# Optimization experiments

Measured on AMD Instinct MI355X. Metric: run time of the kernel, lower is better.

Reference implementation:

```python
import jax, jax.numpy as jnp
import numpy as np

B, T, K, FT, FP, N, H, HEADS, C = 8, 5, 20, 384, 3, 128, 64, 8, 2
ALPHA = 0.2
NEG = -9e15


def gru(x, Wi, Wh, bi, bh):
    # x: [M, L, F] -> (full [M, L, Hd], last [M, Hd]); torch nn.GRU cell math
    Hd = Wh.shape[0]
    gx = jnp.einsum('mlf,fg->mlg', x, Wi) + bi  # precompute input projections

    def step(h, gxt):
        gh = h @ Wh + bh
        xr, xz, xn = jnp.split(gxt, 3, axis=-1)
        hr, hz, hn = jnp.split(gh, 3, axis=-1)
        r = jax.nn.sigmoid(xr + hr)
        z = jax.nn.sigmoid(xz + hz)
        n = jnp.tanh(xn + r * hn)
        h = (1. - z) * n + z * h
        return h, h

    h0 = jnp.zeros((x.shape[0], Hd), x.dtype)
    last, full = jax.lax.scan(step, h0, jnp.swapaxes(gx, 0, 1))
    return jnp.swapaxes(full, 0, 1), last


def temporal_attn(full, last):
    # attend over time using the last hidden state as the query
    a = jax.nn.softmax(jnp.einsum('mlh,mh->ml', full, last), axis=-1)
    return jnp.einsum('ml,mlh->mh', a, full)


def gat_forward(s, p, adj, sm1_Wi, sm1_Wh, sm1_bi, sm1_bh,
                sm2_Wi, sm2_Wh, sm2_bi, sm2_bh,
                pr_Wi, pr_Wh, pr_bi, pr_bh,
                Wb, bb, Wx, bx, W1, a1, W2, a2):
    mask = adj > 0  # [N, N]
    # --- SMEncoder: vectorized over (batch, stock, day) ---
    s_ = jnp.transpose(s, (0, 4, 1, 2, 3)).reshape(B * N * T, K, FT)
    f1, l1 = gru(s_, sm1_Wi, sm1_Wh, sm1_bi, sm1_bh)
    cv = temporal_attn(f1, l1).reshape(B * N, T, H)          # intra-day context
    f2, l2 = gru(cv, sm2_Wi, sm2_Wh, sm2_bi, sm2_bh)
    ct = temporal_attn(f2, l2).reshape(B, N, H)              # inter-day context
    # --- PriceEncoder: vectorized over (batch, stock) ---
    p_ = jnp.transpose(p, (0, 3, 1, 2)).reshape(B * N, T, FP)
    f3, l3 = gru(p_, pr_Wi, pr_Wh, pr_bi, pr_bh)
    qt = temporal_attn(f3, l3).reshape(B, N, H)
    # --- bilinear fusion + per-stock linear head (dropout is eval-mode identity) ---
    X = jnp.tanh(jnp.einsum('bni,oij,bnj->bno', ct, Wb, qt) + bb)   # [B, N, H]
    out1 = jnp.tanh(jnp.einsum('bnh,nch->bnc', X, Wx) + bx)          # [B, N, C]
    # --- multi-head GAT layer 1 (concat + LeakyReLU + adj-masked softmax) ---
    Whd = jnp.einsum('bnh,khf->bknf', X, W1)                         # [B, heads, N, H]
    e = jax.nn.leaky_relu(
        jnp.einsum('bknf,kf->bkn', Whd, a1[:, :H])[:, :, :, None]
        + jnp.einsum('bknf,kf->bkn', Whd, a1[:, H:])[:, :, None, :], ALPHA)
    att = jax.nn.softmax(jnp.where(mask, e, NEG), axis=-1)
    Xh = jax.nn.elu(jnp.einsum('bknm,bkmf->bknf', att, Whd))
    X2 = jnp.transpose(Xh, (0, 2, 1, 3)).reshape(B, N, HEADS * H)    # head concat
    # --- GAT layer 2 -> num_classes ---
    Wh2 = X2 @ W2                                                    # [B, N, C]
    e2 = jax.nn.leaky_relu((Wh2 @ a2[:C])[:, :, None]
                           + (Wh2 @ a2[C:])[:, None, :], ALPHA)
    att2 = jax.nn.softmax(jnp.where(mask, e2, NEG), axis=-1)
    Xo = jnp.einsum('bnm,bmc->bnc', att2, Wh2)
    return jnp.transpose(Xo + out1, (0, 2, 1))                       # [B, C, N]


def setup_inputs():
    key = jax.random.key(0)
    ks = jax.random.split(key, 23)
    g = lambda k, sh, sc=0.05: jax.random.normal(k, sh, jnp.float32) * sc
    adj = (jax.random.uniform(ks[2], (N, N)) < 0.3).astype(jnp.float32)
    adj = jnp.maximum(adj, jnp.eye(N, dtype=jnp.float32))
    return {
        's': jax.random.normal(ks[0], (B, T, K, FT, N), jnp.float32),
        'p': jax.random.normal(ks[1], (B, T, FP, N), jnp.float32),
        'adj': adj,
        'sm1_Wi': g(ks[3], (FT, 3 * H)), 'sm1_Wh': g(ks[4], (H, 3 * H)),
        'sm1_bi': g(ks[5], (3 * H,)), 'sm1_bh': g(ks[6], (3 * H,)),
        'sm2_Wi': g(ks[7], (H, 3 * H)), 'sm2_Wh': g(ks[8], (H, 3 * H)),
        'sm2_bi': g(ks[9], (3 * H,)), 'sm2_bh': g(ks[10], (3 * H,)),
        'pr_Wi': g(ks[11], (FP, 3 * H)), 'pr_Wh': g(ks[12], (H, 3 * H)),
        'pr_bi': g(ks[13], (3 * H,)), 'pr_bh': g(ks[14], (3 * H,)),
        'Wb': g(ks[15], (H, H, H)), 'bb': g(ks[16], (H,)),
        'Wx': g(ks[17], (N, C, H)), 'bx': g(ks[18], (N, C)),
        'W1': g(ks[19], (HEADS, H, H)), 'a1': g(ks[20], (HEADS, 2 * H)),
        'W2': g(ks[21], (HEADS * H, C)), 'a2': g(ks[22], (2 * C,)),
    }


def reference(s, p, adj, sm1_Wi, sm1_Wh, sm1_bi, sm1_bh,
              sm2_Wi, sm2_Wh, sm2_bi, sm2_bh,
              pr_Wi, pr_Wh, pr_bi, pr_bh,
              Wb, bb, Wx, bx, W1, a1, W2, a2):
    return gat_forward(s, p, adj, sm1_Wi, sm1_Wh, sm1_bi, sm1_bh,
                       sm2_Wi, sm2_Wh, sm2_bi, sm2_bh,
                       pr_Wi, pr_Wh, pr_bi, pr_bh,
                       Wb, bb, Wx, bx, W1, a1, W2, a2)
```

## Files before the change

kernel.cpp:

```cpp
#include <hip/hip_runtime.h>
#include <hip/hip_bf16.h>
#include <hip/hip_fp16.h>

#define DI __device__ __forceinline__

namespace {

constexpr int G_  = 192;
constexpr int FT_ = 384;
constexpr int M1_ = 5120;

typedef _Float16 f16x8 __attribute__((ext_vector_type(8)));
typedef _Float16 f16x4 __attribute__((ext_vector_type(4)));
typedef float    f32x4 __attribute__((ext_vector_type(4)));

DI float lrelu(float x) { return x > 0.f ? x : 0.2f * x; }
DI float sigmoidf(float x) { return 1.f / (1.f + __expf(-x)); }
DI float tanh_fast(float x) { float e = __expf(2.f * x); return 1.f - 2.f / (e + 1.f); }

__global__ __launch_bounds__(256) void k_cvtB(
    const float* __restrict__ Wi, _Float16* __restrict__ Bt) {
  int v = blockIdx.x * 256 + threadIdx.x;
  int g = v / 384, f = v % 384;
  Bt[v] = (_Float16)Wi[f * 192 + g];
}

__global__ __launch_bounds__(256) void k_gx1(
    const float* __restrict__ s, const _Float16* __restrict__ Bt,
    const float* __restrict__ bi, __half* __restrict__ gx1) {
  const int slab = blockIdx.x;
  const int b = slab / 100, rem = slab % 100, t = rem / 20, k = rem % 20;
  const float* A = s + (size_t)((b * 5 + t) * 20 + k) * (FT_ * 128);
  __shared__ __align__(16) _Float16 AsL[128 * 40];
  __shared__ __align__(16) _Float16 BsL[192 * 40];
  __shared__ float bisL[192];
  const int tid = threadIdx.x;
  if (tid < 192) bisL[tid] = bi[tid];
  const int w = tid >> 6, l = tid & 63;
  const int lr = l & 15, lk = l >> 4;

  f32x4 acc[12][2];
#pragma unroll
  for (int gt = 0; gt < 12; ++gt)
#pragma unroll
    for (int nt = 0; nt < 2; ++nt) acc[gt][nt] = (f32x4){0.f, 0.f, 0.f, 0.f};

  for (int kc = 0; kc < 12; ++kc) {
    const int f0 = kc * 32;
#pragma unroll
    for (int pass = 0; pass < 2; ++pass) {
      int task = tid + 256 * pass;
      int n = task & 127, oct = task >> 7;
      const float* src = A + (size_t)(f0 + oct * 8) * 128 + n;
      float v[8];
#pragma unroll
      for (int j = 0; j < 8; ++j) v[j] = src[j * 128];
      f16x8 h;
#pragma unroll
      for (int j = 0; j < 8; ++j) h[j] = (_Float16)v[j];
      *(f16x8*)&AsL[n * 40 + oct * 8] = h;
    }
#pragma unroll
    for (int pass = 0; pass < 3; ++pass) {
      int c = tid + 256 * pass;
      int g = c >> 2, oct = c & 3;
      f16x8 h = *(const f16x8*)&Bt[(size_t)g * 384 + f0 + oct * 8];
      *(f16x8*)&BsL[g * 40 + oct * 8] = h;
    }
    __syncthreads();
    f16x8 aN[2];
#pragma unroll
    for (int nt = 0; nt < 2; ++nt)
      aN[nt] = *(const f16x8*)&AsL[(w * 32 + nt * 16 + lr) * 40 + lk * 8];
#pragma unroll
    for (int gt = 0; gt < 12; ++gt) {
      f16x8 bW = *(const f16x8*)&BsL[(gt * 16 + lr) * 40 + lk * 8];
      acc[gt][0] = __builtin_amdgcn_mfma_f32_16x16x32_f16(bW, aN[0], acc[gt][0], 0, 0, 0);
      acc[gt][1] = __builtin_amdgcn_mfma_f32_16x16x32_f16(bW, aN[1], acc[gt][1], 0, 0, 0);
    }
    __syncthreads();
  }
#pragma unroll
  for (int nt = 0; nt < 2; ++nt) {
    int n = w * 32 + nt * 16 + lr;
    size_t m = (size_t)(b * 128 + n) * 5 + t;
    _Float16* dst = (_Float16*)gx1 + ((size_t)k * M1_ + m) * G_;
#pragma unroll
    for (int gt = 0; gt < 12; ++gt) {
      int gq = gt * 16 + lk * 4;
      float4 bias = *(const float4*)&bisL[gq];
      f32x4 c = acc[gt][nt];
      f16x4 h;
      h[0] = (_Float16)(c[0] + bias.x);
      h[1] = (_Float16)(c[1] + bias.y);
      h[2] = (_Float16)(c[2] + bias.z);
      h[3] = (_Float16)(c[3] + bias.w);
      *(f16x4*)&dst[gq] = h;
    }
  }
}

__global__ __launch_bounds__(192) void k_scan1(
    const __half* __restrict__ gx1, const float* __restrict__ Wh,
    const float* __restrict__ bh, float* __restrict__ cv) {
  const int s0 = blockIdx.x * 8;
  const int tid = threadIdx.x;
  __shared__ __align__(16) float hist[8][20][64];
  __shared__ float ghl[8][192];
  __shared__ float dls[8][20], als[8][20];
  float whcol[64];
#pragma unroll
  for (int i = 0; i < 64; ++i) whcol[i] = Wh[i * G_ + tid];
  const float bhg = bh[tid];

  for (int k = 0; k < 20; ++k) {
    if (k == 0) {
#pragma unroll
      for (int ss = 0; ss < 8; ++ss) ghl[ss][tid] = bhg;
    } else {
#pragma unroll
      for (int ss = 0; ss < 8; ++ss) {
        const float4* hq = (const float4*)&hist[ss][k - 1][0];
        float a = 0.f;
#pragma unroll
        for (int q = 0; q < 16; ++q) {
          float4 h4 = hq[q];
          a += h4.x * whcol[4 * q]     + h4.y * whcol[4 * q + 1]
             + h4.z * whcol[4 * q + 2] + h4.w * whcol[4 * q + 3];
        }
        ghl[ss][tid] = a + bhg;
      }
    }
    __syncthreads();
#pragma unroll
    for (int base = 0; base < 512; base += 192) {
      int task = base + tid;
      if (task < 512) {
        int ss = task >> 6, i = task & 63;
        size_t gbase = ((size_t)k * M1_ + (s0 + ss)) * G_;
        float xr = __half2float(gx1[gbase + i]);
        float xz = __half2float(gx1[gbase + 64 + i]);
        float xn = __half2float(gx1[gbase + 128 + i]);
        float hr = ghl[ss][i], hz = ghl[ss][64 + i], hn = ghl[ss][128 + i];
        float r  = sigmoidf(xr + hr);
        float z  = sigmoidf(xz + hz);
        float nn = tanh_fast(xn + r * hn);
        float hp = (k == 0) ? 0.f : hist[ss][k - 1][i];
        hist[ss][k][i] = (1.f - z) * nn + z * hp;
      }
    }
    __syncthreads();
  }
  if (tid < 160) {
    int ss = tid / 20, kk = tid % 20;
    float d = 0.f;
#pragma unroll
    for (int i = 0; i < 64; ++i) d += hist[ss][kk][i] * hist[ss][19][i];
    dls[ss][kk] = d;
  }
  __syncthreads();
  if (tid < 160) {
    int ss = tid / 20, kk = tid % 20;
    float mx = -3.4e38f;
#pragma unroll
    for (int j = 0; j < 20; ++j) mx = fmaxf(mx, dls[ss][j]);
    als[ss][kk] = __expf(dls[ss][kk] - mx);
  }
  __syncthreads();
  for (int idx = tid; idx < 512; idx += 192) {
    int ss = idx >> 6, i = idx & 63;
    float sum = 0.f, a = 0.f;
#pragma unroll
    for (int kk = 0; kk < 20; ++kk) sum += als[ss][kk];
#pragma unroll
    for (int kk = 0; kk < 20; ++kk) a += als[ss][kk] * hist[ss][kk][i];
    cv[(size_t)(s0 + ss) * 64 + i] = a / sum;
  }
}

__global__ __launch_bounds__(192) void k_scan2(
    const float* __restrict__ x, const float* __restrict__ Wi,
    const float* __restrict__ Wh, const float* __restrict__ bi,
    const float* __restrict__ bh, float* __restrict__ outv) {
  const int s0 = blockIdx.x * 4;
  const int tid = threadIdx.x;
  __shared__ __align__(16) float hist[4][5][64];
  __shared__ __align__(16) float xl[4][64];
  __shared__ float ghl[4][192], gxl[4][192];
  __shared__ float dls[4][5], als[4][5];
  float wic[64], whc[64];
#pragma unroll
  for (int i = 0; i < 64; ++i) { wic[i] = Wi[i * G_ + tid]; whc[i] = Wh[i * G_ + tid]; }
  const float big = bi[tid], bhg = bh[tid];

  for (int t = 0; t < 5; ++t) {
    for (int v = tid; v < 256; v += 192) {
      int ss = v >> 6, i = v & 63;
      xl[ss][i] = x[((size_t)(s0 + ss) * 5 + t) * 64 + i];
    }
    __syncthreads();
#pragma unroll
    for (int ss = 0; ss < 4; ++ss) {
      const float4* xq = (const float4*)&xl[ss][0];
      float ax = 0.f;
#pragma unroll
      for (int q = 0; q < 16; ++q) {
        float4 v4 = xq[q];
        ax += v4.x * wic[4 * q]     + v4.y * wic[4 * q + 1]
            + v4.z * wic[4 * q + 2] + v4.w * wic[4 * q + 3];
      }
      gxl[ss][tid] = ax + big;
      float ah = 0.f;
      if (t > 0) {
        const float4* hq = (const float4*)&hist[ss][t - 1][0];
#pragma unroll
        for (int q = 0; q < 16; ++q) {
          float4 h4 = hq[q];
          ah += h4.x * whc[4 * q]     + h4.y * whc[4 * q + 1]
              + h4.z * whc[4 * q + 2] + h4.w * whc[4 * q + 3];
        }
      }
      ghl[ss][tid] = ah + bhg;
    }
    __syncthreads();
    {
      int task = tid;
#pragma unroll
      for (int base = 0; base < 256; base += 192) {
        int tk = base + tid;
        if (tk < 256) {
          int ss = tk >> 6, i = tk & 63;
          float xr = gxl[ss][i], xz = gxl[ss][64 + i], xn = gxl[ss][128 + i];
          float hr = ghl[ss][i], hz = ghl[ss][64 + i], hn = ghl[ss][128 + i];
          float r  = sigmoidf(xr + hr);
          float z  = sigmoidf(xz + hz);
          float nn = tanh_fast(xn + r * hn);
          float hp = (t == 0) ? 0.f : hist[ss][t - 1][i];
          hist[ss][t][i] = (1.f - z) * nn + z * hp;
        }
      }
      (void)task;
    }
    __syncthreads();
  }
  if (tid < 20) {
    int ss = tid / 5, kk = tid % 5;
    float d = 0.f;
#pragma unroll
    for (int i = 0; i < 64; ++i) d += hist[ss][kk][i] * hist[ss][4][i];
    dls[ss][kk] = d;
  }
  __syncthreads();
  if (tid < 20) {
    int ss = tid / 5, kk = tid % 5;
    float mx = -3.4e38f;
#pragma unroll
    for (int j = 0; j < 5; ++j) mx = fmaxf(mx, dls[ss][j]);
    als[ss][kk] = __expf(dls[ss][kk] - mx);
  }
  __syncthreads();
  for (int idx = tid; idx < 256; idx += 192) {
    int ss = idx >> 6, i = idx & 63;
    float sum = 0.f, a = 0.f;
#pragma unroll
    for (int kk = 0; kk < 5; ++kk) sum += als[ss][kk];
#pragma unroll
    for (int kk = 0; kk < 5; ++kk) a += als[ss][kk] * hist[ss][kk][i];
    outv[(size_t)(s0 + ss) * 64 + i] = a / sum;
  }
}

__global__ __launch_bounds__(192) void k_scan3(
    const float* __restrict__ p, const float* __restrict__ Wi,
    const float* __restrict__ Wh, const float* __restrict__ bi,
    const float* __restrict__ bh, float* __restrict__ outv) {
  const int s0 = blockIdx.x * 4;
  const int tid = threadIdx.x;
  __shared__ __align__(16) float hist[4][5][64];
  __shared__ float xp[4][3];
  __shared__ float ghl[4][192], gxl[4][192];
  __shared__ float dls[4][5], als[4][5];
  float wic[3], whc[64];
#pragma unroll
  for (int f = 0; f < 3; ++f) wic[f] = Wi[f * G_ + tid];
#pragma unroll
  for (int i = 0; i < 64; ++i) whc[i] = Wh[i * G_ + tid];
  const float big = bi[tid], bhg = bh[tid];

  for (int t = 0; t < 5; ++t) {
    if (tid < 12) {
      int ss = tid / 3, f = tid % 3;
      int seq = s0 + ss, b = seq >> 7, n = seq & 127;
      xp[ss][f] = p[((size_t)(b * 5 + t) * 3 + f) * 128 + n];
    }
    __syncthreads();
#pragma unroll
    for (int ss = 0; ss < 4; ++ss) {
      gxl[ss][tid] = xp[ss][0] * wic[0] + xp[ss][1] * wic[1] + xp[ss][2] * wic[2] + big;
      float ah = 0.f;
      if (t > 0) {
        const float4* hq = (const float4*)&hist[ss][t - 1][0];
#pragma unroll
        for (int q = 0; q < 16; ++q) {
          float4 h4 = hq[q];
          ah += h4.x * whc[4 * q]     + h4.y * whc[4 * q + 1]
              + h4.z * whc[4 * q + 2] + h4.w * whc[4 * q + 3];
        }
      }
      ghl[ss][tid] = ah + bhg;
    }
    __syncthreads();
#pragma unroll
    for (int base = 0; base < 256; base += 192) {
      int tk = base + tid;
      if (tk < 256) {
        int ss = tk >> 6, i = tk & 63;
        float xr = gxl[ss][i], xz = gxl[ss][64 + i], xn = gxl[ss][128 + i];
        float hr = ghl[ss][i], hz = ghl[ss][64 + i], hn = ghl[ss][128 + i];
        float r  = sigmoidf(xr + hr);
        float z  = sigmoidf(xz + hz);
        float nn = tanh_fast(xn + r * hn);
        float hp = (t == 0) ? 0.f : hist[ss][t - 1][i];
        hist[ss][t][i] = (1.f - z) * nn + z * hp;
      }
    }
    __syncthreads();
  }
  if (tid < 20) {
    int ss = tid / 5, kk = tid % 5;
    float d = 0.f;
#pragma unroll
    for (int i = 0; i < 64; ++i) d += hist[ss][kk][i] * hist[ss][4][i];
    dls[ss][kk] = d;
  }
  __syncthreads();
  if (tid < 20) {
    int ss = tid / 5, kk = tid % 5;
    float mx = -3.4e38f;
#pragma unroll
    for (int j = 0; j < 5; ++j) mx = fmaxf(mx, dls[ss][j]);
    als[ss][kk] = __expf(dls[ss][kk] - mx);
  }
  __syncthreads();
  for (int idx = tid; idx < 256; idx += 192) {
    int ss = idx >> 6, i = idx & 63;
    float sum = 0.f, a = 0.f;
#pragma unroll
    for (int kk = 0; kk < 5; ++kk) sum += als[ss][kk];
#pragma unroll
    for (int kk = 0; kk < 5; ++kk) a += als[ss][kk] * hist[ss][kk][i];
    outv[(size_t)(s0 + ss) * 64 + i] = a / sum;
  }
}

__global__ __launch_bounds__(256) void k_bilinear(
    const float* __restrict__ ct, const float* __restrict__ qt,
    const float* __restrict__ Wb, const float* __restrict__ bb,
    float* __restrict__ X) {
  const int bn0 = blockIdx.x * 4;
  const int tid = threadIdx.x;
  __shared__ float ctl[4][64], qtl[4][64];
  {
    int ss = tid >> 6, i = tid & 63;
    ctl[ss][i] = ct[(size_t)(bn0 + ss) * 64 + i];
    qtl[ss][i] = qt[(size_t)(bn0 + ss) * 64 + i];
  }
  __syncthreads();
  const int o = tid >> 2, part = tid & 3, j0 = part << 4;
  float qr[4][16];
#pragma unroll
  for (int pp = 0; pp < 4; ++pp)
#pragma unroll
    for (int q = 0; q < 16; ++q) qr[pp][q] = qtl[pp][j0 + q];
  float acc[4] = {0.f, 0.f, 0.f, 0.f};
  const float* wb = Wb + (size_t)o * 4096 + j0;
  for (int i = 0; i < 64; ++i) {
    const float4* w4 = (const float4*)(wb + i * 64);
    float tmp[4] = {0.f, 0.f, 0.f, 0.f};
#pragma unroll
    for (int q = 0; q < 4; ++q) {
      float4 w = w4[q];
#pragma unroll
      for (int pp = 0; pp < 4; ++pp)
        tmp[pp] += w.x * qr[pp][4 * q]     + w.y * qr[pp][4 * q + 1]
                 + w.z * qr[pp][4 * q + 2] + w.w * qr[pp][4 * q + 3];
    }
#pragma unroll
    for (int pp = 0; pp < 4; ++pp) acc[pp] += ctl[pp][i] * tmp[pp];
  }
#pragma unroll
  for (int pp = 0; pp < 4; ++pp) {
    acc[pp] += __shfl_xor(acc[pp], 1);
    acc[pp] += __shfl_xor(acc[pp], 2);
  }
  if (part == 0) {
    float bbv = bb[o];
#pragma unroll
    for (int pp = 0; pp < 4; ++pp)
      X[(size_t)(bn0 + pp) * 64 + o] = tanh_fast(acc[pp] + bbv);
  }
}

__global__ __launch_bounds__(256) void k_gat1(
    const float* __restrict__ X, const float* __restrict__ W1,
    const float* __restrict__ a1, const float* __restrict__ adj,
    float* __restrict__ X2) {
  const int b = blockIdx.x >> 3, k = blockIdx.x & 7;
  const int tid = threadIdx.x;
  __shared__ __align__(16) float whd[128][68];
  __shared__ float w1l[64][64];
  __shared__ float d1l[128], d2l[128];
  for (int v = tid; v < 4096; v += 256) w1l[v >> 6][v & 63] = W1[(size_t)k * 4096 + v];
  __syncthreads();
  {
    const int f = tid & 63, ng = tid >> 6;
    const float* Xb = X + (size_t)b * 128 * 64;
    for (int n = ng * 32; n < ng * 32 + 32; ++n) {
      float a = 0.f;
#pragma unroll
      for (int h = 0; h < 64; ++h) a += Xb[n * 64 + h] * w1l[h][f];
      whd[n][f] = a;
    }
  }
  __syncthreads();
  if (tid < 128) {
    const int n = tid;
    float da = 0.f, db = 0.f;
#pragma unroll
    for (int f = 0; f < 64; ++f) {
      float w = whd[n][f];
      da += w * a1[k * 128 + f];
      db += w * a1[k * 128 + 64 + f];
    }
    d1l[n] = da; d2l[n] = db;
  }
  __syncthreads();
  {
    const int n = tid & 127, fh = tid >> 7;
    unsigned long long mlo = 0ull, mhi = 0ull;
    for (int m = 0; m < 64; ++m) if (adj[n * 128 + m] > 0.f)      mlo |= (1ull << m);
    for (int m = 0; m < 64; ++m) if (adj[n * 128 + 64 + m] > 0.f) mhi |= (1ull << m);
    const float d1n = d1l[n];
    float mx = -3.4e38f;
    for (int m = 0; m < 128; ++m) {
      bool on = (m < 64) ? (((mlo >> m) & 1ull) != 0) : (((mhi >> (m - 64)) & 1ull) != 0);
      float e = lrelu(d1n + d2l[m]);
      mx = fmaxf(mx, on ? e : -3.4e38f);
    }
    float sum = 0.f;
    float acc[32];
#pragma unroll
    for (int q = 0; q < 32; ++q) acc[q] = 0.f;
    for (int m = 0; m < 128; ++m) {
      bool on = (m < 64) ? (((mlo >> m) & 1ull) != 0) : (((mhi >> (m - 64)) & 1ull) != 0);
      float w = on ? __expf(lrelu(d1n + d2l[m]) - mx) : 0.f;
      sum += w;
      const float4* wr = (const float4*)&whd[m][fh * 32];
#pragma unroll
      for (int q8 = 0; q8 < 8; ++q8) {
        float4 wv = wr[q8];
        acc[4 * q8]     += w * wv.x;
        acc[4 * q8 + 1] += w * wv.y;
        acc[4 * q8 + 2] += w * wv.z;
        acc[4 * q8 + 3] += w * wv.w;
      }
    }
    float inv = 1.f / sum;
    float* dst = X2 + ((size_t)b * 128 + n) * 512 + k * 64 + fh * 32;
#pragma unroll
    for (int q = 0; q < 32; ++q) {
      float v = acc[q] * inv;
      dst[q] = v > 0.f ? v : (__expf(v) - 1.f);
    }
  }
}

__global__ __launch_bounds__(256) void k_head(
    const float* __restrict__ X, const float* __restrict__ Wx, const float* __restrict__ bx,
    const float* __restrict__ X2, const float* __restrict__ W2, const float* __restrict__ a2,
    const float* __restrict__ adj, float* __restrict__ out) {
  const int b = blockIdx.x;
  const int tid = threadIdx.x;
  __shared__ float w2l[1024];
  __shared__ float wh2l[128][2];
  __shared__ float d2aL[128], d2bL[128];
  __shared__ float out1L[128][2];
  for (int v = tid; v < 1024; v += 256) w2l[v] = W2[v];
  __syncthreads();
  const int w = tid >> 6, l = tid & 63;
  const float a20 = a2[0], a21 = a2[1], a22 = a2[2], a23 = a2[3];
  for (int it = 0; it < 32; ++it) {
    int n = w * 32 + it;
    const float* xr = X2 + ((size_t)b * 128 + n) * 512 + l * 8;
    float4 xa = *(const float4*)xr;
    float4 xb = *(const float4*)(xr + 4);
    float xs[8] = {xa.x, xa.y, xa.z, xa.w, xb.x, xb.y, xb.z, xb.w};
    float s0 = 0.f, s1 = 0.f;
#pragma unroll
    for (int j = 0; j < 8; ++j) {
      s0 += xs[j] * w2l[(l * 8 + j) * 2];
      s1 += xs[j] * w2l[(l * 8 + j) * 2 + 1];
    }
#pragma unroll
    for (int d = 1; d < 64; d <<= 1) { s0 += __shfl_xor(s0, d); s1 += __shfl_xor(s1, d); }
    if (l == 0) {
      wh2l[n][0] = s0; wh2l[n][1] = s1;
      d2aL[n] = s0 * a20 + s1 * a21;
      d2bL[n] = s0 * a22 + s1 * a23;
    }
  }
  if (tid < 128) {
    int n = tid;
    const float* xrow = X + ((size_t)b * 128 + n) * 64;
#pragma unroll
    for (int c = 0; c < 2; ++c) {
      float a = 0.f;
#pragma unroll
      for (int h = 0; h < 64; ++h) a += xrow[h] * Wx[(n * 2 + c) * 64 + h];
      out1L[n][c] = tanh_fast(a + bx[n * 2 + c]);
    }
  }
  __syncthreads();
  if (tid < 128) {
    const int n = tid;
    unsigned long long mlo = 0ull, mhi = 0ull;
    for (int m = 0; m < 64; ++m) if (adj[n * 128 + m] > 0.f)      mlo |= (1ull << m);
    for (int m = 0; m < 64; ++m) if (adj[n * 128 + 64 + m] > 0.f) mhi |= (1ull << m);
    const float dan = d2aL[n];
    float mx = -3.4e38f;
    for (int m = 0; m < 128; ++m) {
      bool on = (m < 64) ? (((mlo >> m) & 1ull) != 0) : (((mhi >> (m - 64)) & 1ull) != 0);
      float e = lrelu(dan + d2bL[m]);
      mx = fmaxf(mx, on ? e : -3.4e38f);
    }
    float sum = 0.f, x0 = 0.f, x1 = 0.f;
    for (int m = 0; m < 128; ++m) {
      bool on = (m < 64) ? (((mlo >> m) & 1ull) != 0) : (((mhi >> (m - 64)) & 1ull) != 0);
      float wgt = on ? __expf(lrelu(dan + d2bL[m]) - mx) : 0.f;
      sum += wgt; x0 += wgt * wh2l[m][0]; x1 += wgt * wh2l[m][1];
    }
    float inv = 1.f / sum;
    out[(size_t)(b * 2 + 0) * 128 + n] = x0 * inv + out1L[n][0];
    out[(size_t)(b * 2 + 1) * 128 + n] = x1 * inv + out1L[n][1];
  }
}

}

extern "C" void kernel_launch(void* const* d_in, const int* in_sizes, int n_in,
                              void* d_out, int out_size, void* d_ws, size_t ws_size,
                              hipStream_t stream) {
  (void)in_sizes; (void)n_in; (void)out_size;
  const float* s      = (const float*)d_in[0];
  const float* p      = (const float*)d_in[1];
  const float* adj    = (const float*)d_in[2];
  const float* sm1_Wi = (const float*)d_in[3];
  const float* sm1_Wh = (const float*)d_in[4];
  const float* sm1_bi = (const float*)d_in[5];
  const float* sm1_bh = (const float*)d_in[6];
  const float* sm2_Wi = (const float*)d_in[7];
  const float* sm2_Wh = (const float*)d_in[8];
  const float* sm2_bi = (const float*)d_in[9];
  const float* sm2_bh = (const float*)d_in[10];
  const float* pr_Wi  = (const float*)d_in[11];
  const float* pr_Wh  = (const float*)d_in[12];
  const float* pr_bi  = (const float*)d_in[13];
  const float* pr_bh  = (const float*)d_in[14];
  const float* Wb     = (const float*)d_in[15];
  const float* bb     = (const float*)d_in[16];
  const float* Wx     = (const float*)d_in[17];
  const float* bx     = (const float*)d_in[18];
  const float* W1     = (const float*)d_in[19];
  const float* a1     = (const float*)d_in[20];
  const float* W2     = (const float*)d_in[21];
  const float* a2     = (const float*)d_in[22];

  if (ws_size < 43515904u) return;
  char* ws = (char*)d_ws;
  __half* gx1 = (__half*)ws;
  float* cv   = (float*)(ws + 39321600);
  float* ct   = (float*)(ws + 40632320);
  float* qt   = (float*)(ws + 40894464);
  float* X    = (float*)(ws + 41156608);
  float* X2   = (float*)(ws + 41418752);
  _Float16* Bt = (_Float16*)(ws + 41418752);

  hipLaunchKernelGGL(k_cvtB,     dim3(288),  dim3(256), 0, stream, sm1_Wi, Bt);
  hipLaunchKernelGGL(k_gx1,      dim3(800),  dim3(256), 0, stream, s, Bt, sm1_bi, gx1);
  hipLaunchKernelGGL(k_scan1,    dim3(640),  dim3(192), 0, stream, gx1, sm1_Wh, sm1_bh, cv);
  hipLaunchKernelGGL(k_scan2,    dim3(256),  dim3(192), 0, stream, cv, sm2_Wi, sm2_Wh, sm2_bi, sm2_bh, ct);
  hipLaunchKernelGGL(k_scan3,    dim3(256),  dim3(192), 0, stream, p, pr_Wi, pr_Wh, pr_bi, pr_bh, qt);
  hipLaunchKernelGGL(k_bilinear, dim3(256),  dim3(256), 0, stream, ct, qt, Wb, bb, X);
  hipLaunchKernelGGL(k_gat1,     dim3(64),   dim3(256), 0, stream, X, W1, a1, adj, X2);
  hipLaunchKernelGGL(k_head,     dim3(8),    dim3(256), 0, stream, X, Wx, bx, X2, W2, a2, adj, (float*)d_out);
}
```

Baseline: 553.4 us.

## Run first GRU recurrence with MFMA per wave using fragment-native gx layout

The first GRU scan now runs as one 64-lane wave per group of 16 sequences. The hidden-to-hidden matmul is done with fp16 MFMA using register-resident Wh fragments, and hidden state is redistributed through a small LDS buffer. The gx projection kernel writes its output directly in the MFMA accumulator fragment layout, so each lane loads its gates with vector loads, and the next step's loads are prefetched. This removes the scalar FMA dot products and block-wide barriers of the old scan, at the cost of fp16 hidden state in the matmul and only 320 single-wave blocks.

Result: faster. 503.3 us (-9.0%).

```diff
diff --git a/kernel.cpp b/kernel.cpp
--- a/kernel.cpp
+++ b/kernel.cpp
@@ -8,7 +8,6 @@
 
 constexpr int G_  = 192;
 constexpr int FT_ = 384;
-constexpr int M1_ = 5120;
 
 typedef _Float16 f16x8 __attribute__((ext_vector_type(8)));
 typedef _Float16 f16x4 __attribute__((ext_vector_type(4)));
@@ -27,13 +26,13 @@
 
 __global__ __launch_bounds__(256) void k_gx1(
     const float* __restrict__ s, const _Float16* __restrict__ Bt,
-    const float* __restrict__ bi, __half* __restrict__ gx1) {
+    const float* __restrict__ bi, _Float16* __restrict__ gx1) {
   const int slab = blockIdx.x;
   const int b = slab / 100, rem = slab % 100, t = rem / 20, k = rem % 20;
   const float* A = s + (size_t)((b * 5 + t) * 20 + k) * (FT_ * 128);
   __shared__ __align__(16) _Float16 AsL[128 * 40];
   __shared__ __align__(16) _Float16 BsL[192 * 40];
-  __shared__ float bisL[192];
+  __shared__ __align__(16) float bisL[192];
   const int tid = threadIdx.x;
   if (tid < 192) bisL[tid] = bi[tid];
   const int w = tid >> 6, l = tid & 63;
@@ -80,102 +79,197 @@
     }
     __syncthreads();
   }
+  const size_t base3 = ((size_t)k * 40 + b * 5 + t) * 8;
 #pragma unroll
   for (int nt = 0; nt < 2; ++nt) {
-    int n = w * 32 + nt * 16 + lr;
-    size_t m = (size_t)(b * 128 + n) * 5 + t;
-    _Float16* dst = (_Float16*)gx1 + ((size_t)k * M1_ + m) * G_;
+    const int ngrp = w * 2 + nt;
+    _Float16* dstbase = gx1 + ((base3 + ngrp) * 3) * 1024 + (size_t)l * 16;
+#pragma unroll
+    for (int gate = 0; gate < 3; ++gate) {
+      f16x8 h0, h1;
+#pragma unroll
+      for (int tq = 0; tq < 4; ++tq) {
+        const int gt = gate * 4 + tq;
+        f32x4 bias = *(const f32x4*)&bisL[gt * 16 + lk * 4];
+        f32x4 c = acc[gt][nt];
+#pragma unroll
+        for (int r = 0; r < 4; ++r) {
+          float v = c[r] + bias[r];
+          if (tq < 2) h0[tq * 4 + r] = (_Float16)v;
+          else        h1[(tq - 2) * 4 + r] = (_Float16)v;
+        }
+      }
+      *(f16x8*)(dstbase + (size_t)gate * 1024) = h0;
+      *(f16x8*)(dstbase + (size_t)gate * 1024 + 8) = h1;
+    }
+  }
+}
+
+__global__ __launch_bounds__(64, 1) void k_scan1m(
+    const _Float16* __restrict__ gx, const float* __restrict__ Wh,
+    const float* __restrict__ bh, float* __restrict__ cv) {
+  const int wv = blockIdx.x;
+  const int b = wv / 40, rem = wv % 40, t = rem / 8, ng = rem % 8;
+  const int l = threadIdx.x;
+  const int seq = l & 15, rg = l >> 4;
+
+  __shared__ __align__(16) _Float16 histL[20][64][24];
+  __shared__ __align__(16) _Float16 red[16][72];
+
+  f16x8 whF[12][2];
+#pragma unroll
+  for (int gt = 0; gt < 12; ++gt)
+#pragma unroll
+    for (int c = 0; c < 2; ++c) {
+      f16x8 h;
+#pragma unroll
+      for (int j = 0; j < 8; ++j)
+        h[j] = (_Float16)Wh[(size_t)(32 * c + rg * 8 + j) * 192 + gt * 16 + seq];
+      whF[gt][c] = h;
+    }
+  f32x4 bhF[12];
+#pragma unroll
+  for (int gt = 0; gt < 12; ++gt)
+    bhF[gt] = *(const f32x4*)&bh[gt * 16 + rg * 4];
+
+  float h16[16];
+#pragma unroll
+  for (int j = 0; j < 16; ++j) h16[j] = 0.f;
+
+#define GXP(kk) (gx + ((((size_t)(kk) * 40 + b * 5 + t) * 8 + ng) * 3) * 1024 + (size_t)l * 16)
+
+  f16x8 gxc[3][2], gxn[3][2];
+  {
+    const _Float16* p0 = GXP(0);
+    const _Float16* p1 = GXP(1);
+#pragma unroll
+    for (int g = 0; g < 3; ++g) {
+      gxc[g][0] = *(const f16x8*)(p0 + g * 1024);
+      gxc[g][1] = *(const f16x8*)(p0 + g * 1024 + 8);
+      gxn[g][0] = *(const f16x8*)(p1 + g * 1024);
+      gxn[g][1] = *(const f16x8*)(p1 + g * 1024 + 8);
+    }
+  }
+
+  f16x8 bf0, bf1;
+  f32x4 acc[12];
+
+#define GATES_AND_H(KCONST_HIST)                                               \
+  {                                                                            \
+    _Float16* hp = &histL[KCONST_HIST][l][0];                                  \
+    f16x8 p0, p1;                                                              \
+    _Pragma("unroll")                                                          \
+    for (int tq = 0; tq < 4; ++tq) {                                           \
+      _Pragma("unroll")                                                        \
+      for (int r = 0; r < 4; ++r) {                                            \
+        const int idx = tq * 4 + r;                                            \
+        float xr = (float)gxc[0][idx >> 3][idx & 7];                           \
+        float xz = (float)gxc[1][idx >> 3][idx & 7];                           \
+        float xn = (float)gxc[2][idx >> 3][idx & 7];                           \
+        float hr = acc[tq][r], hz = acc[4 + tq][r], hnv = acc[8 + tq][r];      \
+        float rr = sigmoidf(xr + hr);                                          \
+        float zz = sigmoidf(xz + hz);                                          \
+        float nn = tanh_fast(xn + rr * hnv);                                   \
+        float hv = (1.f - zz) * nn + zz * h16[idx];                            \
+        h16[idx] = hv;                                                         \
+        if (idx < 8) p0[idx] = (_Float16)hv; else p1[idx - 8] = (_Float16)hv;  \
+      }                                                                        \
+    }                                                                          \
+    *(f16x8*)hp = p0;                                                          \
+    *(f16x8*)(hp + 8) = p1;                                                    \
+  }
+
+#define REDIST()                                                               \
+  {                                                                            \
+    _Pragma("unroll")                                                          \
+    for (int tq = 0; tq < 4; ++tq) {                                           \
+      f16x4 q;                                                                 \
+      q[0] = (_Float16)h16[tq * 4 + 0]; q[1] = (_Float16)h16[tq * 4 + 1];      \
+      q[2] = (_Float16)h16[tq * 4 + 2]; q[3] = (_Float16)h16[tq * 4 + 3];      \
+      *(f16x4*)&red[seq][16 * tq + 4 * rg] = q;                                \
+    }                                                                          \
+    bf0 = *(const f16x8*)&red[seq][8 * rg];                                    \
+    bf1 = *(const f16x8*)&red[seq][32 + 8 * rg];                               \
+  }
+
+#pragma unroll
+  for (int gt = 0; gt < 12; ++gt) acc[gt] = bhF[gt];
+  GATES_AND_H(0)
+  REDIST()
+
+  for (int k = 1; k < 19; ++k) {
+#pragma unroll
+    for (int g = 0; g < 3; ++g) { gxc[g][0] = gxn[g][0]; gxc[g][1] = gxn[g][1]; }
+    const _Float16* pn = GXP(k + 1);
+#pragma unroll
+    for (int g = 0; g < 3; ++g) {
+      gxn[g][0] = *(const f16x8*)(pn + g * 1024);
+      gxn[g][1] = *(const f16x8*)(pn + g * 1024 + 8);
+    }
 #pragma unroll
     for (int gt = 0; gt < 12; ++gt) {
-      int gq = gt * 16 + lk * 4;
-      float4 bias = *(const float4*)&bisL[gq];
-      f32x4 c = acc[gt][nt];
-      f16x4 h;
-      h[0] = (_Float16)(c[0] + bias.x);
-      h[1] = (_Float16)(c[1] + bias.y);
-      h[2] = (_Float16)(c[2] + bias.z);
-      h[3] = (_Float16)(c[3] + bias.w);
-      *(f16x4*)&dst[gq] = h;
-    }
-  }
-}
-
-__global__ __launch_bounds__(192) void k_scan1(
-    const __half* __restrict__ gx1, const float* __restrict__ Wh,
-    const float* __restrict__ bh, float* __restrict__ cv) {
-  const int s0 = blockIdx.x * 8;
-  const int tid = threadIdx.x;
-  __shared__ __align__(16) float hist[8][20][64];
-  __shared__ float ghl[8][192];
-  __shared__ float dls[8][20], als[8][20];
-  float whcol[64];
-#pragma unroll
-  for (int i = 0; i < 64; ++i) whcol[i] = Wh[i * G_ + tid];
-  const float bhg = bh[tid];
-
-  for (int k = 0; k < 20; ++k) {
-    if (k == 0) {
-#pragma unroll
-      for (int ss = 0; ss < 8; ++ss) ghl[ss][tid] = bhg;
-    } else {
-#pragma unroll
-      for (int ss = 0; ss < 8; ++ss) {
-        const float4* hq = (const float4*)&hist[ss][k - 1][0];
-        float a = 0.f;
-#pragma unroll
-        for (int q = 0; q < 16; ++q) {
-          float4 h4 = hq[q];
-          a += h4.x * whcol[4 * q]     + h4.y * whcol[4 * q + 1]
-             + h4.z * whcol[4 * q + 2] + h4.w * whcol[4 * q + 3];
-        }
-        ghl[ss][tid] = a + bhg;
-      }
-    }
-    __syncthreads();
-#pragma unroll
-    for (int base = 0; base < 512; base += 192) {
-      int task = base + tid;
-      if (task < 512) {
-        int ss = task >> 6, i = task & 63;
-        size_t gbase = ((size_t)k * M1_ + (s0 + ss)) * G_;
-        float xr = __half2float(gx1[gbase + i]);
-        float xz = __half2float(gx1[gbase + 64 + i]);
-        float xn = __half2float(gx1[gbase + 128 + i]);
-        float hr = ghl[ss][i], hz = ghl[ss][64 + i], hn = ghl[ss][128 + i];
-        float r  = sigmoidf(xr + hr);
-        float z  = sigmoidf(xz + hz);
-        float nn = tanh_fast(xn + r * hn);
-        float hp = (k == 0) ? 0.f : hist[ss][k - 1][i];
-        hist[ss][k][i] = (1.f - z) * nn + z * hp;
-      }
-    }
-    __syncthreads();
-  }
-  if (tid < 160) {
-    int ss = tid / 20, kk = tid % 20;
-    float d = 0.f;
-#pragma unroll
-    for (int i = 0; i < 64; ++i) d += hist[ss][kk][i] * hist[ss][19][i];
-    dls[ss][kk] = d;
-  }
-  __syncthreads();
-  if (tid < 160) {
-    int ss = tid / 20, kk = tid % 20;
-    float mx = -3.4e38f;
-#pragma unroll
-    for (int j = 0; j < 20; ++j) mx = fmaxf(mx, dls[ss][j]);
-    als[ss][kk] = __expf(dls[ss][kk] - mx);
-  }
-  __syncthreads();
-  for (int idx = tid; idx < 512; idx += 192) {
-    int ss = idx >> 6, i = idx & 63;
-    float sum = 0.f, a = 0.f;
-#pragma unroll
-    for (int kk = 0; kk < 20; ++kk) sum += als[ss][kk];
-#pragma unroll
-    for (int kk = 0; kk < 20; ++kk) a += als[ss][kk] * hist[ss][kk][i];
-    cv[(size_t)(s0 + ss) * 64 + i] = a / sum;
-  }
+      acc[gt] = bhF[gt];
+      acc[gt] = __builtin_amdgcn_mfma_f32_16x16x32_f16(whF[gt][0], bf0, acc[gt], 0, 0, 0);
+      acc[gt] = __builtin_amdgcn_mfma_f32_16x16x32_f16(whF[gt][1], bf1, acc[gt], 0, 0, 0);
+    }
+    GATES_AND_H(k)
+    REDIST()
+  }
+
+#pragma unroll
+  for (int g = 0; g < 3; ++g) { gxc[g][0] = gxn[g][0]; gxc[g][1] = gxn[g][1]; }
+#pragma unroll
+  for (int gt = 0; gt < 12; ++gt) {
+    acc[gt] = bhF[gt];
+    acc[gt] = __builtin_amdgcn_mfma_f32_16x16x32_f16(whF[gt][0], bf0, acc[gt], 0, 0, 0);
+    acc[gt] = __builtin_amdgcn_mfma_f32_16x16x32_f16(whF[gt][1], bf1, acc[gt], 0, 0, 0);
+  }
+  GATES_AND_H(19)
+
+  float d[20];
+#pragma unroll
+  for (int kk = 0; kk < 20; ++kk) {
+    f16x8 a0 = *(const f16x8*)&histL[kk][l][0];
+    f16x8 a1 = *(const f16x8*)&histL[kk][l][8];
+    float p = 0.f;
+#pragma unroll
+    for (int j = 0; j < 8; ++j)
+      p += (float)a0[j] * h16[j] + (float)a1[j] * h16[8 + j];
+    p += __shfl_xor(p, 16);
+    p += __shfl_xor(p, 32);
+    d[kk] = p;
+  }
+  float mx = d[0];
+#pragma unroll
+  for (int kk = 1; kk < 20; ++kk) mx = fmaxf(mx, d[kk]);
+  float sum = 0.f;
+#pragma unroll
+  for (int kk = 0; kk < 20; ++kk) { d[kk] = __expf(d[kk] - mx); sum += d[kk]; }
+  const float inv = 1.f / sum;
+  float av[16];
+#pragma unroll
+  for (int j = 0; j < 16; ++j) av[j] = 0.f;
+#pragma unroll
+  for (int kk = 0; kk < 20; ++kk) {
+    f16x8 a0 = *(const f16x8*)&histL[kk][l][0];
+    f16x8 a1 = *(const f16x8*)&histL[kk][l][8];
+    float wgt = d[kk] * inv;
+#pragma unroll
+    for (int j = 0; j < 8; ++j) {
+      av[j]     += wgt * (float)a0[j];
+      av[8 + j] += wgt * (float)a1[j];
+    }
+  }
+  const int n = ng * 16 + seq;
+  float* dst = cv + ((size_t)(b * 128 + n) * 5 + t) * 64;
+#pragma unroll
+  for (int tq = 0; tq < 4; ++tq) {
+    float4 o = make_float4(av[tq * 4], av[tq * 4 + 1], av[tq * 4 + 2], av[tq * 4 + 3]);
+    *(float4*)&dst[16 * tq + 4 * rg] = o;
+  }
+#undef GXP
+#undef GATES_AND_H
+#undef REDIST
 }
 
 __global__ __launch_bounds__(192) void k_scan2(
@@ -223,23 +317,19 @@
       ghl[ss][tid] = ah + bhg;
     }
     __syncthreads();
-    {
-      int task = tid;
-#pragma unroll
-      for (int base = 0; base < 256; base += 192) {
-        int tk = base + tid;
-        if (tk < 256) {
-          int ss = tk >> 6, i = tk & 63;
-          float xr = gxl[ss][i], xz = gxl[ss][64 + i], xn = gxl[ss][128 + i];
-          float hr = ghl[ss][i], hz = ghl[ss][64 + i], hn = ghl[ss][128 + i];
-          float r  = sigmoidf(xr + hr);
-          float z  = sigmoidf(xz + hz);
-          float nn = tanh_fast(xn + r * hn);
-          float hp = (t == 0) ? 0.f : hist[ss][t - 1][i];
-          hist[ss][t][i] = (1.f - z) * nn + z * hp;
-        }
+#pragma unroll
+    for (int base = 0; base < 256; base += 192) {
+      int tk = base + tid;
+      if (tk < 256) {
+        int ss = tk >> 6, i = tk & 63;
+        float xr = gxl[ss][i], xz = gxl[ss][64 + i], xn = gxl[ss][128 + i];
+        float hr = ghl[ss][i], hz = ghl[ss][64 + i], hn = ghl[ss][128 + i];
+        float r  = sigmoidf(xr + hr);
+        float z  = sigmoidf(xz + hz);
+        float nn = tanh_fast(xn + r * hn);
+        float hp = (t == 0) ? 0.f : hist[ss][t - 1][i];
+        hist[ss][t][i] = (1.f - z) * nn + z * hp;
       }
-      (void)task;
     }
     __syncthreads();
   }
@@ -577,7 +667,7 @@
 
   if (ws_size < 43515904u) return;
   char* ws = (char*)d_ws;
-  __half* gx1 = (__half*)ws;
+  _Float16* gx1 = (_Float16*)ws;
   float* cv   = (float*)(ws + 39321600);
   float* ct   = (float*)(ws + 40632320);
   float* qt   = (float*)(ws + 40894464);
@@ -587,7 +677,7 @@
 
   hipLaunchKernelGGL(k_cvtB,     dim3(288),  dim3(256), 0, stream, sm1_Wi, Bt);
   hipLaunchKernelGGL(k_gx1,      dim3(800),  dim3(256), 0, stream, s, Bt, sm1_bi, gx1);
-  hipLaunchKernelGGL(k_scan1,    dim3(640),  dim3(192), 0, stream, gx1, sm1_Wh, sm1_bh, cv);
+  hipLaunchKernelGGL(k_scan1m,   dim3(320),  dim3(64),  0, stream, gx1, sm1_Wh, sm1_bh, cv);
   hipLaunchKernelGGL(k_scan2,    dim3(256),  dim3(192), 0, stream, cv, sm2_Wi, sm2_Wh, sm2_bi, sm2_bh, ct);
   hipLaunchKernelGGL(k_scan3,    dim3(256),  dim3(192), 0, stream, p, pr_Wi, pr_Wh, pr_bi, pr_bh, qt);
   hipLaunchKernelGGL(k_bilinear, dim3(256),  dim3(256), 0, stream, ct, qt, Wb, bb, X);
```
